# Kernel tuning notes

Measured on AMD Instinct MI355X. Metric: run time of the kernel, lower is better.

## Reference

```python
import jax, jax.numpy as jnp
import numpy as np

N_VOCAB = 8192
N_PAIRS = 8_000_000
INCREMENT_BY = 1.0


def setup_inputs() -> dict:
    key = jax.random.key(0)
    k1, k2 = jax.random.split(key)
    left = jax.random.randint(k1, (N_PAIRS,), 0, N_VOCAB, dtype=jnp.int64 if jax.config.jax_enable_x64 else jnp.int32).astype(jnp.int32)
    right = jax.random.randint(k2, (N_PAIRS,), 0, N_VOCAB, dtype=jnp.int32)
    weight = jnp.zeros((N_VOCAB, N_VOCAB), dtype=jnp.float32)
    return {"left": left, "right": right, "weight": weight}


def reference(left, right, weight):
    # record(): torch's unique(dim=1) + counts-weighted index_put is
    # mathematically identical to a duplicate-accumulating scatter-add of
    # increment_by at each (left, right) pair.
    return weight.at[left, right].add(INCREMENT_BY)
```

## Files before the change

### kernel.cpp

```cpp
#include <hip/hip_runtime.h>
#include <stdint.h>

#define NV 8192
#define NBUCKETS 2048
#define CELLS_PER_BUCKET 32768
#define WORDS_PER_BUCKET 16384
#define SLOT 32
#define P1_BLOCKS 256
#define P1_THREADS 1024
#define OVF_CAP (1u << 18)

__global__ void zero_kernel(unsigned int* __restrict__ p, int n) {
    int i = blockIdx.x * blockDim.x + threadIdx.x;
    if (i < n) p[i] = 0u;
}

__device__ __forceinline__ void p1_put(int l, int r,
                                       uint16_t* skeys, unsigned int* scur,
                                       unsigned int* ovf_cnt, uint2* ovf_list) {
    unsigned int b = ((unsigned int)l) >> 2;
    unsigned int sh = (b & 1u) << 4;
    unsigned int old = atomicAdd(&scur[b >> 1], 1u << sh);
    unsigned int s = (old >> sh) & 0xFFFFu;
    if (s < SLOT) {
        skeys[b * SLOT + s] = (uint16_t)((l & 3) * NV + r);
    } else {
        unsigned int o = atomicAdd(ovf_cnt, 1u);
        if (o < OVF_CAP) ovf_list[o] = make_uint2((unsigned)l, (unsigned)r);
    }
}

__global__ __launch_bounds__(P1_THREADS) void p1_partition(
        const int* __restrict__ left, const int* __restrict__ right, int n,
        uint16_t* __restrict__ keys,
        unsigned int* __restrict__ ovf_cnt, uint2* __restrict__ ovf_list) {
    __shared__ uint16_t skeys[NBUCKETS * SLOT];
    __shared__ unsigned int scur[NBUCKETS / 2];

    uint4* sk4 = (uint4*)skeys;
    for (int i = threadIdx.x; i < (NBUCKETS * SLOT) / 8; i += blockDim.x)
        sk4[i] = make_uint4(~0u, ~0u, ~0u, ~0u);
    for (int i = threadIdx.x; i < NBUCKETS / 2; i += blockDim.x) scur[i] = 0u;
    __syncthreads();

    const int4* l4 = (const int4*)left;
    const int4* r4 = (const int4*)right;
    int n4 = n >> 2;
    int chunk = (n4 + gridDim.x - 1) / gridDim.x;
    int s4 = blockIdx.x * chunk;
    int e4 = min(s4 + chunk, n4);

    for (int i = s4 + threadIdx.x; i < e4; i += blockDim.x) {
        int4 l = l4[i];
        int4 r = r4[i];
        p1_put(l.x, r.x, skeys, scur, ovf_cnt, ovf_list);
        p1_put(l.y, r.y, skeys, scur, ovf_cnt, ovf_list);
        p1_put(l.z, r.z, skeys, scur, ovf_cnt, ovf_list);
        p1_put(l.w, r.w, skeys, scur, ovf_cnt, ovf_list);
    }
    if (blockIdx.x == gridDim.x - 1)
        for (int i = (n4 << 2) + threadIdx.x; i < n; i += blockDim.x)
            p1_put(left[i], right[i], skeys, scur, ovf_cnt, ovf_list);
    __syncthreads();

    uint4* kg = (uint4*)keys;
    size_t base = (size_t)blockIdx.x * ((NBUCKETS * SLOT) / 8);
    for (int i = threadIdx.x; i < (NBUCKETS * SLOT) / 8; i += blockDim.x)
        kg[base + i] = sk4[i];
}

__global__ __launch_bounds__(1024) void p2_accum(
        const uint16_t* __restrict__ keys,
        const float4* __restrict__ w4, float4* __restrict__ out4) {
    __shared__ unsigned int cnt[WORDS_PER_BUCKET];
    int b = blockIdx.x;
    for (int i = threadIdx.x; i < WORDS_PER_BUCKET; i += blockDim.x) cnt[i] = 0u;
    __syncthreads();

    const uint4* k16 = (const uint4*)keys;
    for (int i = threadIdx.x; i < P1_BLOCKS * 4; i += blockDim.x) {
        int blk = i >> 2;
        int q = i & 3;
        uint4 wv = k16[((size_t)blk * NBUCKETS + b) * 4 + q];
        unsigned int ws[4] = {wv.x, wv.y, wv.z, wv.w};
#pragma unroll
        for (int j = 0; j < 4; ++j) {
            unsigned int k0 = ws[j] & 0xFFFFu;
            unsigned int k1 = ws[j] >> 16;
            if (k0 < 32768u) atomicAdd(&cnt[k0 >> 1], 1u << ((k0 & 1u) << 4));
            if (k1 < 32768u) atomicAdd(&cnt[k1 >> 1], 1u << ((k1 & 1u) << 4));
        }
    }
    __syncthreads();

    size_t gbase = (size_t)b * (CELLS_PER_BUCKET / 4);
    for (int i = threadIdx.x; i < CELLS_PER_BUCKET / 4; i += blockDim.x) {
        unsigned int c0 = cnt[2 * i], c1 = cnt[2 * i + 1];
        float4 v = w4[gbase + i];
        v.x += (float)(c0 & 0xFFFFu);
        v.y += (float)(c0 >> 16);
        v.z += (float)(c1 & 0xFFFFu);
        v.w += (float)(c1 >> 16);
        out4[gbase + i] = v;
    }
}

__global__ void ovf_apply(const unsigned int* __restrict__ ovf_cnt,
                          const uint2* __restrict__ ovf_list,
                          float* __restrict__ out) {
    unsigned int m = min(*ovf_cnt, OVF_CAP);
    int idx = blockIdx.x * blockDim.x + threadIdx.x;
    int stride = gridDim.x * blockDim.x;
    for (unsigned int i = idx; i < m; i += stride)
        atomicAdd(&out[(size_t)ovf_list[i].x * NV + ovf_list[i].y], 1.0f);
}

__global__ void fb_copy_kernel(const float4* __restrict__ w,
                               float4* __restrict__ out, int n4) {
    int idx = blockIdx.x * blockDim.x + threadIdx.x;
    int stride = gridDim.x * blockDim.x;
    for (int i = idx; i < n4; i += stride) out[i] = w[i];
}
__global__ void fb_scatter_kernel(const int* __restrict__ left,
                                  const int* __restrict__ right,
                                  float* __restrict__ out, int n) {
    int idx = blockIdx.x * blockDim.x + threadIdx.x;
    int stride = gridDim.x * blockDim.x;
    for (int i = idx; i < n; i += stride)
        atomicAdd(&out[(size_t)left[i] * NV + right[i]], 1.0f);
}

extern "C" void kernel_launch(void* const* d_in, const int* in_sizes, int n_in,
                              void* d_out, int out_size, void* d_ws, size_t ws_size,
                              hipStream_t stream) {
    const int* left  = (const int*)d_in[0];
    const int* right = (const int*)d_in[1];
    const float* w   = (const float*)d_in[2];
    float* out = (float*)d_out;
    int n = in_sizes[0];

    size_t keysBytes = (size_t)P1_BLOCKS * NBUCKETS * SLOT * 2;
    size_t ovcBytes  = 256;
    size_t ovfBytes  = (size_t)OVF_CAP * 8;
    size_t needed = keysBytes + ovcBytes + ovfBytes;

    if (n > 0 && ws_size >= needed) {
        uint8_t* p = (uint8_t*)d_ws;
        uint16_t* keys        = (uint16_t*)p;      p += keysBytes;
        unsigned int* ovf_cnt = (unsigned int*)p;  p += ovcBytes;
        uint2* ovf_list       = (uint2*)p;

        zero_kernel <<<1, 64, 0, stream>>>(ovf_cnt, 1);
        p1_partition<<<P1_BLOCKS, P1_THREADS, 0, stream>>>(left, right, n,
                                                           keys, ovf_cnt, ovf_list);
        p2_accum    <<<NBUCKETS, 1024, 0, stream>>>(keys,
                                                    (const float4*)w, (float4*)out);
        ovf_apply   <<<32, 256, 0, stream>>>(ovf_cnt, ovf_list, out);
    } else {
        int nv4 = out_size / 4;
        fb_copy_kernel<<<4096, 256, 0, stream>>>((const float4*)w, (float4*)out, nv4);
        if (n > 0)
            fb_scatter_kernel<<<2048, 256, 0, stream>>>(left, right, out, n);
    }
}
```

Baseline: 141.3 us.

## Use per-block shared overflow lists, halve slots, double partition blocks, nontemporal accum IO

The partition pass now runs 512 blocks with 16 key slots per bucket, so each block uses much less LDS and more blocks can be resident per CU. Overflowing pairs go to a per-block shared-memory list that is flushed to a per-block global region, instead of contending on one global atomic counter. This also removes the separate zeroing kernel launch. The accumulate pass reads the weight matrix and writes the output with nontemporal builtins to cut cache pollution on the large streaming traffic. In exchange, overflow is more frequent with the smaller slots, it is silently dropped past 512 entries per block, and the overflow apply step is serialized per thread.

```diff
diff --git a/kernel.cpp b/kernel.cpp
--- a/kernel.cpp
+++ b/kernel.cpp
@@ -5,19 +5,16 @@
 #define NBUCKETS 2048
 #define CELLS_PER_BUCKET 32768
 #define WORDS_PER_BUCKET 16384
-#define SLOT 32
-#define P1_BLOCKS 256
+#define SLOT 16
+#define P1_BLOCKS 512
 #define P1_THREADS 1024
-#define OVF_CAP (1u << 18)
+#define OVB 512
 
-__global__ void zero_kernel(unsigned int* __restrict__ p, int n) {
-    int i = blockIdx.x * blockDim.x + threadIdx.x;
-    if (i < n) p[i] = 0u;
-}
+typedef float f32x4 __attribute__((ext_vector_type(4)));
 
 __device__ __forceinline__ void p1_put(int l, int r,
                                        uint16_t* skeys, unsigned int* scur,
-                                       unsigned int* ovf_cnt, uint2* ovf_list) {
+                                       unsigned int* sobc, uint2* sovf) {
     unsigned int b = ((unsigned int)l) >> 2;
     unsigned int sh = (b & 1u) << 4;
     unsigned int old = atomicAdd(&scur[b >> 1], 1u << sh);
@@ -25,22 +22,26 @@
     if (s < SLOT) {
         skeys[b * SLOT + s] = (uint16_t)((l & 3) * NV + r);
     } else {
-        unsigned int o = atomicAdd(ovf_cnt, 1u);
-        if (o < OVF_CAP) ovf_list[o] = make_uint2((unsigned)l, (unsigned)r);
+        unsigned int o = atomicAdd(sobc, 1u);
+        if (o < OVB) sovf[o] = make_uint2((unsigned)l, (unsigned)r);
     }
 }
 
 __global__ __launch_bounds__(P1_THREADS) void p1_partition(
         const int* __restrict__ left, const int* __restrict__ right, int n,
         uint16_t* __restrict__ keys,
-        unsigned int* __restrict__ ovf_cnt, uint2* __restrict__ ovf_list) {
+        uint2* __restrict__ ovf,
+        unsigned int* __restrict__ ovf_cnt) {
     __shared__ uint16_t skeys[NBUCKETS * SLOT];
     __shared__ unsigned int scur[NBUCKETS / 2];
+    __shared__ uint2 sovf[OVB];
+    __shared__ unsigned int sobc;
 
     uint4* sk4 = (uint4*)skeys;
     for (int i = threadIdx.x; i < (NBUCKETS * SLOT) / 8; i += blockDim.x)
         sk4[i] = make_uint4(~0u, ~0u, ~0u, ~0u);
     for (int i = threadIdx.x; i < NBUCKETS / 2; i += blockDim.x) scur[i] = 0u;
+    if (threadIdx.x == 0) sobc = 0u;
     __syncthreads();
 
     const int4* l4 = (const int4*)left;
@@ -53,35 +54,40 @@
     for (int i = s4 + threadIdx.x; i < e4; i += blockDim.x) {
         int4 l = l4[i];
         int4 r = r4[i];
-        p1_put(l.x, r.x, skeys, scur, ovf_cnt, ovf_list);
-        p1_put(l.y, r.y, skeys, scur, ovf_cnt, ovf_list);
-        p1_put(l.z, r.z, skeys, scur, ovf_cnt, ovf_list);
-        p1_put(l.w, r.w, skeys, scur, ovf_cnt, ovf_list);
+        p1_put(l.x, r.x, skeys, scur, &sobc, sovf);
+        p1_put(l.y, r.y, skeys, scur, &sobc, sovf);
+        p1_put(l.z, r.z, skeys, scur, &sobc, sovf);
+        p1_put(l.w, r.w, skeys, scur, &sobc, sovf);
     }
     if (blockIdx.x == gridDim.x - 1)
         for (int i = (n4 << 2) + threadIdx.x; i < n; i += blockDim.x)
-            p1_put(left[i], right[i], skeys, scur, ovf_cnt, ovf_list);
+            p1_put(left[i], right[i], skeys, scur, &sobc, sovf);
     __syncthreads();
 
     uint4* kg = (uint4*)keys;
     size_t base = (size_t)blockIdx.x * ((NBUCKETS * SLOT) / 8);
     for (int i = threadIdx.x; i < (NBUCKETS * SLOT) / 8; i += blockDim.x)
         kg[base + i] = sk4[i];
+
+    unsigned int oc = min(sobc, (unsigned int)OVB);
+    for (unsigned int i = threadIdx.x; i < oc; i += blockDim.x)
+        ovf[(size_t)blockIdx.x * OVB + i] = sovf[i];
+    if (threadIdx.x == 0) ovf_cnt[blockIdx.x] = oc;
 }
 
 __global__ __launch_bounds__(1024) void p2_accum(
         const uint16_t* __restrict__ keys,
-        const float4* __restrict__ w4, float4* __restrict__ out4) {
+        const f32x4* __restrict__ w4, f32x4* __restrict__ out4) {
     __shared__ unsigned int cnt[WORDS_PER_BUCKET];
     int b = blockIdx.x;
     for (int i = threadIdx.x; i < WORDS_PER_BUCKET; i += blockDim.x) cnt[i] = 0u;
     __syncthreads();
 
     const uint4* k16 = (const uint4*)keys;
-    for (int i = threadIdx.x; i < P1_BLOCKS * 4; i += blockDim.x) {
-        int blk = i >> 2;
-        int q = i & 3;
-        uint4 wv = k16[((size_t)blk * NBUCKETS + b) * 4 + q];
+    for (int i = threadIdx.x; i < P1_BLOCKS * 2; i += blockDim.x) {
+        int blk = i >> 1;
+        int q = i & 1;
+        uint4 wv = k16[((size_t)blk * NBUCKETS + b) * 2 + q];
         unsigned int ws[4] = {wv.x, wv.y, wv.z, wv.w};
 #pragma unroll
         for (int j = 0; j < 4; ++j) {
@@ -96,23 +102,24 @@
     size_t gbase = (size_t)b * (CELLS_PER_BUCKET / 4);
     for (int i = threadIdx.x; i < CELLS_PER_BUCKET / 4; i += blockDim.x) {
         unsigned int c0 = cnt[2 * i], c1 = cnt[2 * i + 1];
-        float4 v = w4[gbase + i];
+        f32x4 v = __builtin_nontemporal_load(&w4[gbase + i]);
         v.x += (float)(c0 & 0xFFFFu);
         v.y += (float)(c0 >> 16);
         v.z += (float)(c1 & 0xFFFFu);
         v.w += (float)(c1 >> 16);
-        out4[gbase + i] = v;
+        __builtin_nontemporal_store(v, &out4[gbase + i]);
     }
 }
 
-__global__ void ovf_apply(const unsigned int* __restrict__ ovf_cnt,
-                          const uint2* __restrict__ ovf_list,
+__global__ void ovf_apply(const uint2* __restrict__ ovf,
+                          const unsigned int* __restrict__ ovf_cnt,
                           float* __restrict__ out) {
-    unsigned int m = min(*ovf_cnt, OVF_CAP);
-    int idx = blockIdx.x * blockDim.x + threadIdx.x;
-    int stride = gridDim.x * blockDim.x;
-    for (unsigned int i = idx; i < m; i += stride)
-        atomicAdd(&out[(size_t)ovf_list[i].x * NV + ovf_list[i].y], 1.0f);
+    int blk = blockIdx.x * blockDim.x + threadIdx.x;
+    if (blk >= P1_BLOCKS) return;
+    unsigned int m = ovf_cnt[blk];
+    const uint2* lst = ovf + (size_t)blk * OVB;
+    for (unsigned int i = 0; i < m; ++i)
+        atomicAdd(&out[(size_t)lst[i].x * NV + lst[i].y], 1.0f);
 }
 
 __global__ void fb_copy_kernel(const float4* __restrict__ w,
@@ -140,22 +147,21 @@
     int n = in_sizes[0];
 
     size_t keysBytes = (size_t)P1_BLOCKS * NBUCKETS * SLOT * 2;
-    size_t ovcBytes  = 256;
-    size_t ovfBytes  = (size_t)OVF_CAP * 8;
-    size_t needed = keysBytes + ovcBytes + ovfBytes;
+    size_t ovfBytes  = (size_t)P1_BLOCKS * OVB * 8;
+    size_t ovcBytes  = ((size_t)P1_BLOCKS * 4 + 255) & ~(size_t)255;
+    size_t needed = keysBytes + ovfBytes + ovcBytes;
 
     if (n > 0 && ws_size >= needed) {
         uint8_t* p = (uint8_t*)d_ws;
         uint16_t* keys        = (uint16_t*)p;      p += keysBytes;
-        unsigned int* ovf_cnt = (unsigned int*)p;  p += ovcBytes;
-        uint2* ovf_list       = (uint2*)p;
+        uint2* ovf            = (uint2*)p;         p += ovfBytes;
+        unsigned int* ovf_cnt = (unsigned int*)p;
 
-        zero_kernel <<<1, 64, 0, stream>>>(ovf_cnt, 1);
         p1_partition<<<P1_BLOCKS, P1_THREADS, 0, stream>>>(left, right, n,
-                                                           keys, ovf_cnt, ovf_list);
+                                                           keys, ovf, ovf_cnt);
         p2_accum    <<<NBUCKETS, 1024, 0, stream>>>(keys,
-                                                    (const float4*)w, (float4*)out);
-        ovf_apply   <<<32, 256, 0, stream>>>(ovf_cnt, ovf_list, out);
+                                                    (const f32x4*)w, (f32x4*)out);
+        ovf_apply   <<<(P1_BLOCKS + 255) / 256, 256, 0, stream>>>(ovf, ovf_cnt, out);
     } else {
         int nv4 = out_size / 4;
         fb_copy_kernel<<<4096, 256, 0, stream>>>((const float4*)w, (float4*)out, nv4);
```

New measurement: 144.6 us. +2.4%, slower.
